# Performance work log

Measured on AMD Instinct MI355X. Metric: run time of the kernel, lower is better.

Reference implementation:

```python
import jax, jax.numpy as jnp
import numpy as np

S, B, H, V, U = 512, 16, 256, 10000, 10000
LAMBDA_T = 0.1   # flashback default temporal decay
LAMBDA_S = 100.0 # flashback default spatial decay
DAY = 86400.0


def setup_inputs() -> dict:
    key = jax.random.key(0)
    ks = jax.random.split(key, 16)
    x = jax.random.randint(ks[0], (S, B), 0, V)
    t = jax.random.uniform(ks[1], (S, B), jnp.float32) * (7.0 * DAY)  # timestamps in seconds
    s = jax.random.normal(ks[2], (S, B, 2), jnp.float32)              # lat/lon-like coords
    y_t = jax.random.uniform(ks[3], (S, B), jnp.float32)
    y_s = jax.random.normal(ks[4], (S, B, 2), jnp.float32)
    h = jnp.zeros((2, B, H), jnp.float32)
    active_user = jax.random.randint(ks[5], (1, B), 0, U)
    sc = 0.02
    enc_emb = jax.random.normal(ks[6], (V, H), jnp.float32) * sc
    user_emb = jax.random.normal(ks[7], (U, H), jnp.float32) * sc
    Wih_f = jax.random.normal(ks[8], (H, H), jnp.float32) * sc
    Whh_f = jax.random.normal(ks[9], (H, H), jnp.float32) * sc
    b_f = jnp.zeros((H,), jnp.float32)
    Wih_b = jax.random.normal(ks[10], (H, H), jnp.float32) * sc
    Whh_b = jax.random.normal(ks[11], (H, H), jnp.float32) * sc
    b_b = jnp.zeros((H,), jnp.float32)
    fc_W = jax.random.normal(ks[12], (V, 3 * H), jnp.float32) * sc
    fc_b = jnp.zeros((V,), jnp.float32)
    return dict(x=x, t=t, s=s, y_t=y_t, y_s=y_s, h=h, active_user=active_user,
                enc_emb=enc_emb, user_emb=user_emb,
                Wih_f=Wih_f, Whh_f=Whh_f, b_f=b_f,
                Wih_b=Wih_b, Whh_b=Whh_b, b_b=b_b,
                fc_W=fc_W, fc_b=fc_b)


def _rnn_dir(xe, h0, Wih, Whh, b):
    # vanilla tanh RNN over leading (time) axis; xe: [S,B,H]
    def step(hprev, xt):
        hn = jnp.tanh(xt @ Wih.T + hprev @ Whh.T + b)
        return hn, hn
    hT, ys = jax.lax.scan(step, h0, xe)
    return ys, hT


def _forward(x, t, s, h, active_user, enc_emb, user_emb,
             Wih_f, Whh_f, b_f, Wih_b, Whh_b, b_b, fc_W, fc_b):
    seq_len, user_len = x.shape
    x_emb = enc_emb[x]                           # [S,B,H]
    out_f, h_f = _rnn_dir(x_emb, h[0], Wih_f, Whh_f, b_f)
    out_b_rev, h_b = _rnn_dir(x_emb[::-1], h[1], Wih_b, Whh_b, b_b)
    h_out = jnp.stack([h_f, h_b], 0)             # [2,B,H]

    # pairwise causal decay weights (i = query step, j = key step, j <= i)
    dt = t[:, None, :] - t[None, :, :]           # [S,S,B]
    ds = jnp.sqrt(jnp.sum((s[:, None] - s[None, :]) ** 2, axis=-1))  # [S,S,B]
    a = ((jnp.cos(dt * (2.0 * np.pi / DAY)) + 1.0) * 0.5) * jnp.exp(-(dt / DAY) * LAMBDA_T)
    b_w = jnp.exp(-ds * LAMBDA_S)
    w = a * b_w + 1e-10                          # [S,S,B]
    causal = jnp.tril(jnp.ones((seq_len, seq_len), w.dtype))
    w = w * causal[:, :, None]
    sum_w = jnp.sum(w, axis=1)                   # [S,B]
    out_w_forward = jnp.einsum('ijb,jbh->ibh', w, out_f) / sum_w[:, :, None]
    # NOTE: original code has a bug (accumulates out_w_backward into itself),
    # so out_w_backward is identically zero; reproduce faithfully.
    out_w_backward = jnp.zeros_like(out_w_forward)

    out_w = jnp.concatenate([out_w_forward, out_w_backward], axis=2)  # [S,B,2H]
    ow = jnp.transpose(out_w, (1, 0, 2))         # [B,S,2H]
    # dropout is identity in eval mode -> query == out_w
    scores = jnp.einsum('bqd,bkd->bqk', ow, ow) / jnp.sqrt(jnp.asarray(2 * H, ow.dtype))
    alpha = jax.nn.softmax(scores, axis=-1)
    ctx = jnp.einsum('bqk,bkd->bqd', alpha, ow)  # [B,S,2H]
    attn_output = jnp.transpose(ctx, (1, 0, 2))  # [S,B,2H]

    p_u = user_emb[active_user.reshape(user_len)]            # [B,H]
    p_u_b = jnp.broadcast_to(p_u[None], (seq_len, user_len, H))
    out_pu = jnp.concatenate([attn_output, p_u_b], axis=2)   # [S,B,3H]
    y_linear = out_pu @ fc_W.T + fc_b                        # [S,B,V]
    return y_linear, h_out


def reference(x, t, s, y_t, y_s, h, active_user, enc_emb, user_emb,
              Wih_f, Whh_f, b_f, Wih_b, Whh_b, b_b, fc_W, fc_b):
    return _forward(x, t, s, h, active_user, enc_emb, user_emb,
                    Wih_f, Whh_f, b_f, Wih_b, Whh_b, b_b, fc_W, fc_b)
```

## Files before the change

### kernel.cpp

```cpp
#include <hip/hip_runtime.h>

typedef unsigned short ushort_t;
typedef __attribute__((ext_vector_type(8))) short short8;
typedef __attribute__((ext_vector_type(4))) float f32x4;

#define S_LEN 512
#define NB 16
#define NH 256
#define NV 10000

__device__ __forceinline__ unsigned short f2bf(float f){
  unsigned u = __float_as_uint(f);
  u += 0x7fffu + ((u >> 16) & 1u);
  return (unsigned short)(u >> 16);
}


__global__ __launch_bounds__(256) void k_prep_xemb(const int* __restrict__ x,
    const float* __restrict__ emb, ushort_t* __restrict__ xe, ushort_t* __restrict__ xer){
  int g = blockIdx.x * 256 + threadIdx.x;
  int m = g >> 5, c = (g & 31) << 3;
  int xm = x[m];
  const float* src = emb + (size_t)xm * NH + c;
  float4 a = *(const float4*)src, b = *(const float4*)(src + 4);
  union { ushort_t us[8]; uint4 v; } u;
  u.us[0]=f2bf(a.x); u.us[1]=f2bf(a.y); u.us[2]=f2bf(a.z); u.us[3]=f2bf(a.w);
  u.us[4]=f2bf(b.x); u.us[5]=f2bf(b.y); u.us[6]=f2bf(b.z); u.us[7]=f2bf(b.w);
  int s = m >> 4, bidx = m & 15;
  int mr = ((S_LEN - 1 - s) << 4) | bidx;
  *(uint4*)&xe [(size_t)m  * NH + c] = u.v;
  *(uint4*)&xer[(size_t)mr * NH + c] = u.v;
}

__global__ __launch_bounds__(256) void k_cvt(const float* __restrict__ src,
                                             ushort_t* __restrict__ dst, int n){
  int g = (blockIdx.x * 256 + threadIdx.x) * 8;
  if (g >= n) return;
  float4 a = *(const float4*)(src + g), b = *(const float4*)(src + g + 4);
  union { ushort_t us[8]; uint4 v; } u;
  u.us[0]=f2bf(a.x); u.us[1]=f2bf(a.y); u.us[2]=f2bf(a.z); u.us[3]=f2bf(a.w);
  u.us[4]=f2bf(b.x); u.us[5]=f2bf(b.y); u.us[6]=f2bf(b.z); u.us[7]=f2bf(b.w);
  *(uint4*)&dst[g] = u.v;
}

__global__ __launch_bounds__(256) void k_prep_fcw(const float* __restrict__ fcW,
                                                  ushort_t* __restrict__ out){
  int g = blockIdx.x * 256 + threadIdx.x;
  int v = g >> 5, c = (g & 31) << 3;
  union { ushort_t us[8]; uint4 q; } u;
  if (v < NV){
    const float* p = fcW + (size_t)v * 768 + c;
    float4 a = *(const float4*)p, b = *(const float4*)(p + 4);
    u.us[0]=f2bf(a.x); u.us[1]=f2bf(a.y); u.us[2]=f2bf(a.z); u.us[3]=f2bf(a.w);
    u.us[4]=f2bf(b.x); u.us[5]=f2bf(b.y); u.us[6]=f2bf(b.z); u.us[7]=f2bf(b.w);
  } else {
    u.q = make_uint4(0,0,0,0);
  }
  *(uint4*)&out[(size_t)v * NH + c] = u.q;
}

__global__ __launch_bounds__(256) void k_prep_tsT(const float* __restrict__ t,
    const float* __restrict__ s2, float* __restrict__ tT,
    float* __restrict__ sxT, float* __restrict__ syT){
  int g = blockIdx.x * 256 + threadIdx.x;
  int j = g >> 4, b = g & 15;
  tT [b * S_LEN + j] = t[g];
  sxT[b * S_LEN + j] = s2[(size_t)g * 2];
  syT[b * S_LEN + j] = s2[(size_t)g * 2 + 1];
}

__global__ __launch_bounds__(256) void k_prep_w(const float* __restrict__ tT,
    const float* __restrict__ sxT, const float* __restrict__ syT,
    ushort_t* __restrict__ wb, float* __restrict__ rsum){
  int i = blockIdx.x, b = blockIdx.y, tid = threadIdx.x;
  const float C1 = 7.272205216643040e-05f;
  const float C2 = -1.1574074074074074e-06f;
  float ti = tT[b*S_LEN+i], sxi = sxT[b*S_LEN+i], syi = syT[b*S_LEN+i];
  __shared__ float red[256];
  float psum = 0.f;
  #pragma unroll
  for (int u2 = 0; u2 < 2; u2++){
    int j = tid + u2 * 256;
    float w = 0.f;
    if (j <= i){
      float dt = ti - tT[b*S_LEN+j];
      float dx = sxi - sxT[b*S_LEN+j], dy = syi - syT[b*S_LEN+j];
      float ds = sqrtf(dx*dx + dy*dy);
      float a = (__cosf(dt * C1) + 1.f) * 0.5f * __expf(dt * C2);
      float bw = __expf(-100.f * ds);
      w = a * bw + 1e-10f;
    }
    psum += w;
    wb[((size_t)b * S_LEN + i) * S_LEN + j] = f2bf(w);
  }
  red[tid] = psum; __syncthreads();
  for (int st = 128; st > 0; st >>= 1){
    if (tid < st) red[tid] += red[tid + st];
    __syncthreads();
  }
  if (tid == 0) rsum[b * S_LEN + i] = 1.f / red[0];
}

__global__ __launch_bounds__(256) void k_ulog(const int* __restrict__ au,
    const float* __restrict__ uemb, const float* __restrict__ fcW,
    const float* __restrict__ fcb, float* __restrict__ ulog){
  __shared__ float pl[16 * 256];
  int tid = threadIdx.x;
  for (int idx = tid; idx < 16 * 256; idx += 256){
    int b = idx >> 8, hc = idx & 255;
    pl[idx] = uemb[(size_t)au[b] * NH + hc];
  }
  __syncthreads();
  int v = blockIdx.x * 256 + tid;
  if (v >= NV) return;
  float acc[16];
  #pragma unroll
  for (int b = 0; b < 16; b++) acc[b] = 0.f;
  const float* wrow = fcW + (size_t)v * 768 + 512;
  for (int hc = 0; hc < 256; hc += 4){
    float4 w4 = *(const float4*)(wrow + hc);
    #pragma unroll
    for (int b = 0; b < 16; b++){
      acc[b] += w4.x * pl[b*256+hc] + w4.y * pl[b*256+hc+1]
              + w4.z * pl[b*256+hc+2] + w4.w * pl[b*256+hc+3];
    }
  }
  float fb = fcb[v];
  #pragma unroll
  for (int b = 0; b < 16; b++) ulog[(size_t)b * NV + v] = acc[b] + fb;
}

__global__ __launch_bounds__(256) void k_transpose(const ushort_t* __restrict__ src,
    ushort_t* __restrict__ dst, int R, int C, long long sstride, long long dstride){
  __shared__ ushort_t tile[32][33];
  int z = blockIdx.z;
  int c0 = blockIdx.x * 32, r0 = blockIdx.y * 32;
  int tx = threadIdx.x & 31, ty = threadIdx.x >> 5;
  const ushort_t* Sp = src + (size_t)sstride * z;
  ushort_t* Dp = dst + (size_t)dstride * z;
  #pragma unroll
  for (int i = 0; i < 32; i += 8) tile[ty+i][tx] = Sp[(size_t)(r0+ty+i) * C + c0 + tx];
  __syncthreads();
  #pragma unroll
  for (int i = 0; i < 32; i += 8) Dp[(size_t)(c0+ty+i) * R + r0 + tx] = tile[tx][ty+i];
}

__global__ __launch_bounds__(256, 2) void k_gemm(
    const ushort_t* __restrict__ A, const ushort_t* __restrict__ Bt, void* __restrict__ Cp,
    int M, int N, int K, int lda, int ldb, int ldc,
    long long sAz, long long sBz, long long sCz,
    const float* __restrict__ bias,
    const float* __restrict__ rowscale, int rsStride,
    const float* __restrict__ addrow, int ldu,
    float cscale, int cmode){
  __shared__ __align__(16) ushort_t As[128 * 40];
  __shared__ __align__(16) ushort_t Bs[128 * 40];
  int z = blockIdx.z;
  int n0 = blockIdx.x * 128, m0 = blockIdx.y * 128;
  int tid = threadIdx.x;
  int wave = tid >> 6, lane = tid & 63;
  int l15 = lane & 15, q4 = lane >> 4;
  int wm = (wave >> 1) * 64, wn = (wave & 1) * 64;
  const ushort_t* Ab = A + (size_t)sAz * z;
  const ushort_t* Bb = Bt + (size_t)sBz * z;
  int srow = tid >> 1, scol = (tid & 1) * 16;
  f32x4 acc[4][4];
  #pragma unroll
  for (int tm = 0; tm < 4; tm++)
    #pragma unroll
    for (int tn = 0; tn < 4; tn++) acc[tm][tn] = (f32x4){0.f,0.f,0.f,0.f};

  for (int k0 = 0; k0 < K; k0 += 32){
    __syncthreads();
    const ushort_t* ap = Ab + (size_t)(m0+srow)*lda + k0 + scol;
    const ushort_t* bp = Bb + (size_t)(n0+srow)*ldb + k0 + scol;
    *(uint4*)&As[srow*40 + scol]     = *(const uint4*)ap;
    *(uint4*)&As[srow*40 + scol + 8] = *(const uint4*)(ap + 8);
    *(uint4*)&Bs[srow*40 + scol]     = *(const uint4*)bp;
    *(uint4*)&Bs[srow*40 + scol + 8] = *(const uint4*)(bp + 8);
    __syncthreads();
    short8 af[4], bf[4];
    #pragma unroll
    for (int tm = 0; tm < 4; tm++) af[tm] = *(const short8*)&As[(wm + tm*16 + l15)*40 + q4*8];
    #pragma unroll
    for (int tn = 0; tn < 4; tn++) bf[tn] = *(const short8*)&Bs[(wn + tn*16 + l15)*40 + q4*8];
    #pragma unroll
    for (int tm = 0; tm < 4; tm++)
      #pragma unroll
      for (int tn = 0; tn < 4; tn++)
        acc[tm][tn] = __builtin_amdgcn_mfma_f32_16x16x32_bf16(af[tm], bf[tn], acc[tm][tn], 0, 0, 0);
  }

  #pragma unroll
  for (int tm = 0; tm < 4; tm++)
    #pragma unroll
    for (int tn = 0; tn < 4; tn++)
      #pragma unroll
      for (int r = 0; r < 4; r++){
        int mr = m0 + wm + tm*16 + q4*4 + r;
        int nc = n0 + wn + tn*16 + l15;
        if (nc < N){
          float v = acc[tm][tn][r] * cscale;
          if (bias)     v += bias[nc];
          if (rowscale) v *= rowscale[(size_t)z * rsStride + mr];
          if (addrow)   v += addrow[(size_t)(mr & 15) * ldu + nc];
          if (cmode == 0){
            ((float*)Cp)[(size_t)sCz * z + (size_t)mr * ldc + nc] = v;
          } else if (cmode == 1){
            ((ushort_t*)Cp)[(size_t)sCz * z + (size_t)mr * ldc + nc] = f2bf(v);
          } else {
            ((ushort_t*)Cp)[((size_t)mr * 16 + z) * ldc + nc] = f2bf(v);
          }
        }
      }
}

__global__ __launch_bounds__(512, 1) void k_rnn(
    const float* __restrict__ WhhF, const float* __restrict__ WhhB,
    const float* __restrict__ xWf, const float* __restrict__ xWb,
    const float* __restrict__ h0,
    ushort_t* __restrict__ outf,
    float* __restrict__ hout){
  int dir = blockIdx.x >> 1, half = blockIdx.x & 1;
  const float* Whh = dir ? WhhB : WhhF;
  const float* xW  = dir ? xWb : xWf;
  int tid = threadIdx.x, wave = tid >> 6, lane = tid & 63;
  int l15 = lane & 15, q4 = lane >> 4;
  __shared__ __align__(16) ushort_t hl[2][8 * 264];

  for (int idx = tid; idx < 2048; idx += 512){
    int m = idx >> 8, n = idx & 255;
    hl[0][m*264 + n] = f2bf(h0[((size_t)dir * 16 + half * 8 + m) * NH + n]);
  }

  short8 bfr[2][8];
  #pragma unroll
  for (int tn = 0; tn < 2; tn++)
    #pragma unroll
    for (int kk = 0; kk < 8; kk++){
      int n = wave*32 + tn*16 + l15;
      int k = kk*32 + q4*8;
      const float* wp = Whh + (size_t)n * NH + k;
      float4 wa = *(const float4*)wp, wb2 = *(const float4*)(wp + 4);
      short8 f;
      f[0]=(short)f2bf(wa.x); f[1]=(short)f2bf(wa.y); f[2]=(short)f2bf(wa.z); f[3]=(short)f2bf(wa.w);
      f[4]=(short)f2bf(wb2.x); f[5]=(short)f2bf(wb2.y); f[6]=(short)f2bf(wb2.z); f[7]=(short)f2bf(wb2.w);
      bfr[tn][kk] = f;
    }

  int myTn = q4 >> 1;
  int mb   = (q4 & 1) * 4;
  int ncol = wave*32 + myTn*16 + l15;

  const float* xwp = xW + (size_t)(half*8 + mb) * NH + ncol;
  float xwE[4], xwO[4];
  #pragma unroll
  for (int r = 0; r < 4; r++){
    xwE[r] = xwp[r * 256];
    xwO[r] = xwp[r * 256 + 16 * 256];
  }
  xwp += 2 * 16 * 256;

  ushort_t* outp0 = outf + (size_t)(half*8 + mb) * 512 * NH + ncol;
  ushort_t* outp1 = outp0 + (size_t)512 * NH;
  ushort_t* outp2 = outp1 + (size_t)512 * NH;
  ushort_t* outp3 = outp2 + (size_t)512 * NH;

  __syncthreads();

#define RNN_STEP(S_, RB_, WB_, XWU_)                                              \
  {                                                                               \
    short8 af[8];                                                                 \
    _Pragma("unroll")                                                             \
    for (int kk = 0; kk < 8; kk++)                                                \
      af[kk] = *(const short8*)&hl[RB_][(lane & 7)*264 + kk*32 + q4*8];           \
    f32x4 acc0 = (f32x4){0.f,0.f,0.f,0.f}, acc1 = acc0;                           \
    _Pragma("unroll")                                                             \
    for (int kk = 0; kk < 8; kk++){                                               \
      acc0 = __builtin_amdgcn_mfma_f32_16x16x32_bf16(af[kk], bfr[0][kk], acc0, 0,0,0); \
      acc1 = __builtin_amdgcn_mfma_f32_16x16x32_bf16(af[kk], bfr[1][kk], acc1, 0,0,0); \
    }                                                                             \
    f32x4 accS = myTn ? acc1 : acc0;                                              \
    float hv[4];                                                                  \
    _Pragma("unroll")                                                             \
    for (int r = 0; r < 4; r++){                                                  \
      float pre = accS[r] + XWU_[r];                                              \
      float ex = __expf(2.f * pre);                                               \
      hv[r] = 1.f - 2.f * __builtin_amdgcn_rcpf(ex + 1.f);                        \
      hl[WB_][(mb + r)*264 + ncol] = f2bf(hv[r]);                                 \
    }                                                                             \
    if (dir == 0){                                                                \
      outp0[0] = f2bf(hv[0]); outp1[0] = f2bf(hv[1]);                             \
      outp2[0] = f2bf(hv[2]); outp3[0] = f2bf(hv[3]);                             \
      outp0 += 256; outp1 += 256; outp2 += 256; outp3 += 256;                     \
    }                                                                             \
    if ((S_) == 511){                                                             \
      _Pragma("unroll")                                                           \
      for (int r = 0; r < 4; r++)                                                 \
        hout[((size_t)dir*16 + half*8 + mb + r) * NH + ncol] = hv[r];             \
    }                                                                             \
    if ((S_) < 510){                                                              \
      _Pragma("unroll")                                                           \
      for (int r = 0; r < 4; r++) XWU_[r] = xwp[r * 256];                         \
      xwp += 16 * 256;                                                            \
    }                                                                             \
    asm volatile("s_waitcnt lgkmcnt(0)" ::: "memory");                            \
    __builtin_amdgcn_s_barrier();                                                 \
    asm volatile("" ::: "memory");                                                \
  }

  for (int s = 0; s < 512; s += 2){
    RNN_STEP(s,     0, 1, xwE)
    RNN_STEP(s + 1, 1, 0, xwO)
  }
#undef RNN_STEP
}

__global__ __launch_bounds__(256) void k_softmax(const float* __restrict__ sc,
                                                 ushort_t* __restrict__ alpha){
  int q = blockIdx.x, z = blockIdx.y, tid = threadIdx.x;
  const float* row = sc + ((size_t)z * S_LEN + q) * S_LEN;
  float v0 = row[tid], v1 = row[tid + 256];
  __shared__ float red[256];
  red[tid] = fmaxf(v0, v1); __syncthreads();
  for (int st = 128; st > 0; st >>= 1){
    if (tid < st) red[tid] = fmaxf(red[tid], red[tid + st]);
    __syncthreads();
  }
  float mx = red[0]; __syncthreads();
  float e0 = __expf(v0 - mx), e1 = __expf(v1 - mx);
  red[tid] = e0 + e1; __syncthreads();
  for (int st = 128; st > 0; st >>= 1){
    if (tid < st) red[tid] += red[tid + st];
    __syncthreads();
  }
  float inv = 1.f / red[0];
  ushort_t* arow = alpha + ((size_t)z * S_LEN + q) * S_LEN;
  arow[tid]       = f2bf(e0 * inv);
  arow[tid + 256] = f2bf(e1 * inv);
}

extern "C" void kernel_launch(void* const* d_in, const int* in_sizes, int n_in,
                              void* d_out, int out_size, void* d_ws, size_t ws_size,
                              hipStream_t stream){
  const int*   x    = (const int*)d_in[0];
  const float* t    = (const float*)d_in[1];
  const float* s2   = (const float*)d_in[2];
  const float* h0   = (const float*)d_in[5];
  const int*   au   = (const int*)d_in[6];
  const float* emb  = (const float*)d_in[7];
  const float* uemb = (const float*)d_in[8];
  const float* WihF = (const float*)d_in[9];
  const float* WhhF = (const float*)d_in[10];
  const float* bF   = (const float*)d_in[11];
  const float* WihB = (const float*)d_in[12];
  const float* WhhB = (const float*)d_in[13];
  const float* bB   = (const float*)d_in[14];
  const float* fcW  = (const float*)d_in[15];
  const float* fcb  = (const float*)d_in[16];
  float* y    = (float*)d_out;
  float* hout = y + (size_t)S_LEN * NB * NV;

  char* wsc = (char*)d_ws;
  size_t off = 0;
  auto alloc = [&](size_t bytes) -> void* {
    void* p = wsc + off;
    off += (bytes + 255) & ~(size_t)255;
    return p;
  };
  ushort_t* xe    = (ushort_t*)alloc(8192 * 256 * 2);
  ushort_t* xer   = (ushort_t*)alloc(8192 * 256 * 2);
  ushort_t* wihf  = (ushort_t*)alloc(256 * 256 * 2);
  ushort_t* wihb  = (ushort_t*)alloc(256 * 256 * 2);
  float*    xwf   = (float*)alloc((size_t)8192 * 256 * 4);
  float*    xwb   = (float*)alloc((size_t)8192 * 256 * 4);
  ushort_t* outf  = (ushort_t*)alloc((size_t)16 * 512 * 256 * 2);
  ushort_t* outfT = (ushort_t*)alloc((size_t)16 * 256 * 512 * 2);
  ushort_t* wbuf  = (ushort_t*)alloc((size_t)16 * 512 * 512 * 2);
  float*    rsum  = (float*)alloc(16 * 512 * 4);
  ushort_t* owf   = (ushort_t*)alloc((size_t)16 * 512 * 256 * 2);
  ushort_t* owfT  = (ushort_t*)alloc((size_t)16 * 256 * 512 * 2);
  ushort_t* fcw1  = (ushort_t*)alloc((size_t)10112 * 256 * 2);
  float*    ulog  = (float*)alloc((size_t)16 * NV * 4);
  float*    tT    = (float*)alloc(16 * 512 * 4);
  float*    sxT   = (float*)alloc(16 * 512 * 4);
  float*    syT   = (float*)alloc(16 * 512 * 4);
  ushort_t* ctx   = (ushort_t*)alloc((size_t)8192 * 256 * 2);
  float*    scores = xwf;
  ushort_t* alpha  = wbuf;

  k_prep_xemb<<<dim3(1024), dim3(256), 0, stream>>>(x, emb, xe, xer);
  k_cvt<<<dim3(32), dim3(256), 0, stream>>>(WihF, wihf, 65536);
  k_cvt<<<dim3(32), dim3(256), 0, stream>>>(WihB, wihb, 65536);
  k_prep_fcw<<<dim3(1264), dim3(256), 0, stream>>>(fcW, fcw1);
  k_prep_tsT<<<dim3(32), dim3(256), 0, stream>>>(t, s2, tT, sxT, syT);
  k_prep_w<<<dim3(512, 16), dim3(256), 0, stream>>>(tT, sxT, syT, wbuf, rsum);
  k_ulog<<<dim3(40), dim3(256), 0, stream>>>(au, uemb, fcW, fcb, ulog);

  k_gemm<<<dim3(2, 64, 1), dim3(256), 0, stream>>>(xe, wihf, xwf,
      8192, 256, 256, 256, 256, 256, 0, 0, 0, bF, nullptr, 0, nullptr, 0, 1.f, 0);
  k_gemm<<<dim3(2, 64, 1), dim3(256), 0, stream>>>(xer, wihb, xwb,
      8192, 256, 256, 256, 256, 256, 0, 0, 0, bB, nullptr, 0, nullptr, 0, 1.f, 0);

  k_rnn<<<dim3(4), dim3(512), 0, stream>>>(WhhF, WhhB, xwf, xwb, h0, outf, hout);

  k_transpose<<<dim3(8, 16, 16), dim3(256), 0, stream>>>(outf, outfT, 512, 256,
      (long long)512 * 256, (long long)256 * 512);

  k_gemm<<<dim3(2, 4, 16), dim3(256), 0, stream>>>(wbuf, outfT, owf,
      512, 256, 512, 512, 512, 256,
      (long long)512 * 512, (long long)256 * 512, (long long)512 * 256,
      nullptr, rsum, 512, nullptr, 0, 1.f, 1);
  k_transpose<<<dim3(8, 16, 16), dim3(256), 0, stream>>>(owf, owfT, 512, 256,
      (long long)512 * 256, (long long)256 * 512);

  k_gemm<<<dim3(4, 4, 16), dim3(256), 0, stream>>>(owf, owf, scores,
      512, 512, 256, 256, 256, 512,
      (long long)512 * 256, (long long)512 * 256, (long long)512 * 512,
      nullptr, nullptr, 0, nullptr, 0, 0.04419417382415922f, 0);

  k_softmax<<<dim3(512, 16), dim3(256), 0, stream>>>(scores, alpha);

  k_gemm<<<dim3(2, 4, 16), dim3(256), 0, stream>>>(alpha, owfT, ctx,
      512, 256, 512, 512, 512, 256,
      (long long)512 * 512, (long long)256 * 512, 0,
      nullptr, nullptr, 0, nullptr, 0, 1.f, 2);

  k_gemm<<<dim3(79, 64, 1), dim3(256), 0, stream>>>(ctx, fcw1, y,
      8192, 10000, 256, 256, 256, 10000, 0, 0, 0,
      nullptr, nullptr, 0, ulog, 10000, 1.f, 0);
}
```

Baseline: 966.1 us.

## Overlap prep work with serial RNN by fusing into one launch

The serial 4-block RNN kernel now shares a launch with the fc-weight conversion, decay-weight construction and user-embedding conversion blocks, so those independent jobs can fill idle CUs while the recurrence runs. The RNN waves get raised priority and the MFMA accumulation is split into two chains to shorten dependency latency. The user-logit term moves from a scalar FP32 kernel to the bf16 MFMA GEMM, which needs an added row bound check. Buffers are reused (fcw2 aliases xe, pu aliases wihf), so correctness depends on ordering, and the prep blocks may compete with the RNN blocks for resources.

```diff
diff --git a/kernel.cpp b/kernel.cpp
--- a/kernel.cpp
+++ b/kernel.cpp
@@ -15,119 +15,35 @@
   return (unsigned short)(u >> 16);
 }
 
-
-__global__ __launch_bounds__(256) void k_prep_xemb(const int* __restrict__ x,
-    const float* __restrict__ emb, ushort_t* __restrict__ xe, ushort_t* __restrict__ xer){
-  int g = blockIdx.x * 256 + threadIdx.x;
-  int m = g >> 5, c = (g & 31) << 3;
-  int xm = x[m];
-  const float* src = emb + (size_t)xm * NH + c;
-  float4 a = *(const float4*)src, b = *(const float4*)(src + 4);
-  union { ushort_t us[8]; uint4 v; } u;
-  u.us[0]=f2bf(a.x); u.us[1]=f2bf(a.y); u.us[2]=f2bf(a.z); u.us[3]=f2bf(a.w);
-  u.us[4]=f2bf(b.x); u.us[5]=f2bf(b.y); u.us[6]=f2bf(b.z); u.us[7]=f2bf(b.w);
-  int s = m >> 4, bidx = m & 15;
-  int mr = ((S_LEN - 1 - s) << 4) | bidx;
-  *(uint4*)&xe [(size_t)m  * NH + c] = u.v;
-  *(uint4*)&xer[(size_t)mr * NH + c] = u.v;
-}
-
-__global__ __launch_bounds__(256) void k_cvt(const float* __restrict__ src,
-                                             ushort_t* __restrict__ dst, int n){
-  int g = (blockIdx.x * 256 + threadIdx.x) * 8;
-  if (g >= n) return;
+__global__ __launch_bounds__(512) void k_prep0(const int* __restrict__ x,
+    const float* __restrict__ emb, ushort_t* __restrict__ xe, ushort_t* __restrict__ xer,
+    const float* __restrict__ WihF, ushort_t* __restrict__ wihf,
+    const float* __restrict__ WihB, ushort_t* __restrict__ wihb){
+  int bx = blockIdx.x, tid = threadIdx.x;
+  if (bx < 512){
+    int g = bx * 512 + tid;
+    int m = g >> 5, c = (g & 31) << 3;
+    int xm = x[m];
+    const float* src = emb + (size_t)xm * NH + c;
+    float4 a = *(const float4*)src, b = *(const float4*)(src + 4);
+    union { ushort_t us[8]; uint4 v; } u;
+    u.us[0]=f2bf(a.x); u.us[1]=f2bf(a.y); u.us[2]=f2bf(a.z); u.us[3]=f2bf(a.w);
+    u.us[4]=f2bf(b.x); u.us[5]=f2bf(b.y); u.us[6]=f2bf(b.z); u.us[7]=f2bf(b.w);
+    int s = m >> 4, bidx = m & 15;
+    int mr = ((S_LEN - 1 - s) << 4) | bidx;
+    *(uint4*)&xe [(size_t)m  * NH + c] = u.v;
+    *(uint4*)&xer[(size_t)mr * NH + c] = u.v;
+    return;
+  }
+  bx -= 512;
+  const float* src = (bx < 16) ? WihF : WihB;
+  ushort_t* dst = (bx < 16) ? wihf : wihb;
+  int g = ((bx & 15) * 512 + tid) * 8;
   float4 a = *(const float4*)(src + g), b = *(const float4*)(src + g + 4);
   union { ushort_t us[8]; uint4 v; } u;
   u.us[0]=f2bf(a.x); u.us[1]=f2bf(a.y); u.us[2]=f2bf(a.z); u.us[3]=f2bf(a.w);
   u.us[4]=f2bf(b.x); u.us[5]=f2bf(b.y); u.us[6]=f2bf(b.z); u.us[7]=f2bf(b.w);
   *(uint4*)&dst[g] = u.v;
-}
-
-__global__ __launch_bounds__(256) void k_prep_fcw(const float* __restrict__ fcW,
-                                                  ushort_t* __restrict__ out){
-  int g = blockIdx.x * 256 + threadIdx.x;
-  int v = g >> 5, c = (g & 31) << 3;
-  union { ushort_t us[8]; uint4 q; } u;
-  if (v < NV){
-    const float* p = fcW + (size_t)v * 768 + c;
-    float4 a = *(const float4*)p, b = *(const float4*)(p + 4);
-    u.us[0]=f2bf(a.x); u.us[1]=f2bf(a.y); u.us[2]=f2bf(a.z); u.us[3]=f2bf(a.w);
-    u.us[4]=f2bf(b.x); u.us[5]=f2bf(b.y); u.us[6]=f2bf(b.z); u.us[7]=f2bf(b.w);
-  } else {
-    u.q = make_uint4(0,0,0,0);
-  }
-  *(uint4*)&out[(size_t)v * NH + c] = u.q;
-}
-
-__global__ __launch_bounds__(256) void k_prep_tsT(const float* __restrict__ t,
-    const float* __restrict__ s2, float* __restrict__ tT,
-    float* __restrict__ sxT, float* __restrict__ syT){
-  int g = blockIdx.x * 256 + threadIdx.x;
-  int j = g >> 4, b = g & 15;
-  tT [b * S_LEN + j] = t[g];
-  sxT[b * S_LEN + j] = s2[(size_t)g * 2];
-  syT[b * S_LEN + j] = s2[(size_t)g * 2 + 1];
-}
-
-__global__ __launch_bounds__(256) void k_prep_w(const float* __restrict__ tT,
-    const float* __restrict__ sxT, const float* __restrict__ syT,
-    ushort_t* __restrict__ wb, float* __restrict__ rsum){
-  int i = blockIdx.x, b = blockIdx.y, tid = threadIdx.x;
-  const float C1 = 7.272205216643040e-05f;
-  const float C2 = -1.1574074074074074e-06f;
-  float ti = tT[b*S_LEN+i], sxi = sxT[b*S_LEN+i], syi = syT[b*S_LEN+i];
-  __shared__ float red[256];
-  float psum = 0.f;
-  #pragma unroll
-  for (int u2 = 0; u2 < 2; u2++){
-    int j = tid + u2 * 256;
-    float w = 0.f;
-    if (j <= i){
-      float dt = ti - tT[b*S_LEN+j];
-      float dx = sxi - sxT[b*S_LEN+j], dy = syi - syT[b*S_LEN+j];
-      float ds = sqrtf(dx*dx + dy*dy);
-      float a = (__cosf(dt * C1) + 1.f) * 0.5f * __expf(dt * C2);
-      float bw = __expf(-100.f * ds);
-      w = a * bw + 1e-10f;
-    }
-    psum += w;
-    wb[((size_t)b * S_LEN + i) * S_LEN + j] = f2bf(w);
-  }
-  red[tid] = psum; __syncthreads();
-  for (int st = 128; st > 0; st >>= 1){
-    if (tid < st) red[tid] += red[tid + st];
-    __syncthreads();
-  }
-  if (tid == 0) rsum[b * S_LEN + i] = 1.f / red[0];
-}
-
-__global__ __launch_bounds__(256) void k_ulog(const int* __restrict__ au,
-    const float* __restrict__ uemb, const float* __restrict__ fcW,
-    const float* __restrict__ fcb, float* __restrict__ ulog){
-  __shared__ float pl[16 * 256];
-  int tid = threadIdx.x;
-  for (int idx = tid; idx < 16 * 256; idx += 256){
-    int b = idx >> 8, hc = idx & 255;
-    pl[idx] = uemb[(size_t)au[b] * NH + hc];
-  }
-  __syncthreads();
-  int v = blockIdx.x * 256 + tid;
-  if (v >= NV) return;
-  float acc[16];
-  #pragma unroll
-  for (int b = 0; b < 16; b++) acc[b] = 0.f;
-  const float* wrow = fcW + (size_t)v * 768 + 512;
-  for (int hc = 0; hc < 256; hc += 4){
-    float4 w4 = *(const float4*)(wrow + hc);
-    #pragma unroll
-    for (int b = 0; b < 16; b++){
-      acc[b] += w4.x * pl[b*256+hc] + w4.y * pl[b*256+hc+1]
-              + w4.z * pl[b*256+hc+2] + w4.w * pl[b*256+hc+3];
-    }
-  }
-  float fb = fcb[v];
-  #pragma unroll
-  for (int b = 0; b < 16; b++) ulog[(size_t)b * NV + v] = acc[b] + fb;
 }
 
 __global__ __launch_bounds__(256) void k_transpose(const ushort_t* __restrict__ src,
@@ -199,7 +115,7 @@
       for (int r = 0; r < 4; r++){
         int mr = m0 + wm + tm*16 + q4*4 + r;
         int nc = n0 + wn + tn*16 + l15;
-        if (nc < N){
+        if (nc < N && mr < M){
           float v = acc[tm][tn][r] * cscale;
           if (bias)     v += bias[nc];
           if (rowscale) v *= rowscale[(size_t)z * rsStride + mr];
@@ -215,18 +131,89 @@
       }
 }
 
-__global__ __launch_bounds__(512, 1) void k_rnn(
+__global__ __launch_bounds__(512, 1) void k_fused(
     const float* __restrict__ WhhF, const float* __restrict__ WhhB,
     const float* __restrict__ xWf, const float* __restrict__ xWb,
     const float* __restrict__ h0,
     ushort_t* __restrict__ outf,
-    float* __restrict__ hout){
-  int dir = blockIdx.x >> 1, half = blockIdx.x & 1;
+    float* __restrict__ hout,
+    const float* __restrict__ fcW, ushort_t* __restrict__ fcw1, ushort_t* __restrict__ fcw2,
+    const float* __restrict__ t, const float* __restrict__ s2,
+    ushort_t* __restrict__ wb, float* __restrict__ rsum,
+    const int* __restrict__ au, const float* __restrict__ uemb, ushort_t* __restrict__ pu){
+  __shared__ __align__(16) ushort_t hl[2][8 * 264];
+  int bx = blockIdx.x, tid = threadIdx.x;
+
+  if (bx >= 4){
+    int pb = bx - 4;
+    if (pb < 632){
+      int g = pb * 512 + tid;
+      int v = g >> 5, c = (g & 31) << 3;
+      union { ushort_t us[8]; uint4 q; } u1, u2;
+      if (v < NV){
+        const float* p1 = fcW + (size_t)v * 768 + c;
+        const float* p2 = p1 + 512;
+        float4 a1 = *(const float4*)p1, b1 = *(const float4*)(p1 + 4);
+        float4 a2 = *(const float4*)p2, b2 = *(const float4*)(p2 + 4);
+        u1.us[0]=f2bf(a1.x); u1.us[1]=f2bf(a1.y); u1.us[2]=f2bf(a1.z); u1.us[3]=f2bf(a1.w);
+        u1.us[4]=f2bf(b1.x); u1.us[5]=f2bf(b1.y); u1.us[6]=f2bf(b1.z); u1.us[7]=f2bf(b1.w);
+        u2.us[0]=f2bf(a2.x); u2.us[1]=f2bf(a2.y); u2.us[2]=f2bf(a2.z); u2.us[3]=f2bf(a2.w);
+        u2.us[4]=f2bf(b2.x); u2.us[5]=f2bf(b2.y); u2.us[6]=f2bf(b2.z); u2.us[7]=f2bf(b2.w);
+      } else {
+        u1.q = make_uint4(0,0,0,0); u2.q = u1.q;
+      }
+      *(uint4*)&fcw1[(size_t)v * NH + c] = u1.q;
+      *(uint4*)&fcw2[(size_t)v * NH + c] = u2.q;
+      return;
+    }
+    pb -= 632;
+    if (pb < 8192){
+      float* red = (float*)hl;
+      int i = pb >> 4, b = pb & 15, j = tid;
+      const float C1 = 7.272205216643040e-05f;
+      const float C2 = -1.1574074074074074e-06f;
+      float ti  = t[i*16 + b];
+      float sxi = s2[(size_t)(i*16 + b) * 2], syi = s2[(size_t)(i*16 + b) * 2 + 1];
+      float w = 0.f;
+      if (j <= i){
+        float dt = ti - t[j*16 + b];
+        float dx = sxi - s2[(size_t)(j*16 + b) * 2];
+        float dy = syi - s2[(size_t)(j*16 + b) * 2 + 1];
+        float ds = sqrtf(dx*dx + dy*dy);
+        float a = (__cosf(dt * C1) + 1.f) * 0.5f * __expf(dt * C2);
+        float bw = __expf(-100.f * ds);
+        w = a * bw + 1e-10f;
+      }
+      wb[((size_t)b * S_LEN + i) * S_LEN + j] = f2bf(w);
+      red[j] = w; __syncthreads();
+      for (int st = 256; st > 0; st >>= 1){
+        if (j < st) red[j] += red[j + st];
+        __syncthreads();
+      }
+      if (j == 0) rsum[b * S_LEN + i] = 1.f / red[0];
+      return;
+    }
+    pb -= 8192;
+    int g = pb * 512 + tid;
+    int r = g >> 5, c = (g & 31) << 3;
+    union { ushort_t us[8]; uint4 q; } u;
+    if (r < 16){
+      const float* p = uemb + (size_t)au[r] * NH + c;
+      float4 a = *(const float4*)p, b2 = *(const float4*)(p + 4);
+      u.us[0]=f2bf(a.x); u.us[1]=f2bf(a.y); u.us[2]=f2bf(a.z); u.us[3]=f2bf(a.w);
+      u.us[4]=f2bf(b2.x); u.us[5]=f2bf(b2.y); u.us[6]=f2bf(b2.z); u.us[7]=f2bf(b2.w);
+    } else {
+      u.q = make_uint4(0,0,0,0);
+    }
+    *(uint4*)&pu[(size_t)r * NH + c] = u.q;
+    return;
+  }
+
+  int dir = bx >> 1, half = bx & 1;
   const float* Whh = dir ? WhhB : WhhF;
   const float* xW  = dir ? xWb : xWf;
-  int tid = threadIdx.x, wave = tid >> 6, lane = tid & 63;
+  int wave = tid >> 6, lane = tid & 63;
   int l15 = lane & 15, q4 = lane >> 4;
-  __shared__ __align__(16) ushort_t hl[2][8 * 264];
 
   for (int idx = tid; idx < 2048; idx += 512){
     int m = idx >> 8, n = idx & 255;
@@ -266,6 +253,7 @@
   ushort_t* outp2 = outp1 + (size_t)512 * NH;
   ushort_t* outp3 = outp2 + (size_t)512 * NH;
 
+  __builtin_amdgcn_s_setprio(1);
   __syncthreads();
 
 #define RNN_STEP(S_, RB_, WB_, XWU_)                                              \
@@ -274,13 +262,18 @@
     _Pragma("unroll")                                                             \
     for (int kk = 0; kk < 8; kk++)                                                \
       af[kk] = *(const short8*)&hl[RB_][(lane & 7)*264 + kk*32 + q4*8];           \
-    f32x4 acc0 = (f32x4){0.f,0.f,0.f,0.f}, acc1 = acc0;                           \
+    f32x4 a0a = (f32x4){0.f,0.f,0.f,0.f}, a0b = a0a, a1a = a0a, a1b = a0a;        \
     _Pragma("unroll")                                                             \
-    for (int kk = 0; kk < 8; kk++){                                               \
-      acc0 = __builtin_amdgcn_mfma_f32_16x16x32_bf16(af[kk], bfr[0][kk], acc0, 0,0,0); \
-      acc1 = __builtin_amdgcn_mfma_f32_16x16x32_bf16(af[kk], bfr[1][kk], acc1, 0,0,0); \
-    }                                                                             \
-    f32x4 accS = myTn ? acc1 : acc0;                                              \
+    for (int kk = 0; kk < 4; kk++){                                               \
+      a0a = __builtin_amdgcn_mfma_f32_16x16x32_bf16(af[kk], bfr[0][kk], a0a, 0,0,0); \
+      a1a = __builtin_amdgcn_mfma_f32_16x16x32_bf16(af[kk], bfr[1][kk], a1a, 0,0,0); \
+    }                                                                             \
+    _Pragma("unroll")                                                             \
+    for (int kk = 4; kk < 8; kk++){                                               \
+      a0b = __builtin_amdgcn_mfma_f32_16x16x32_bf16(af[kk], bfr[0][kk], a0b, 0,0,0); \
+      a1b = __builtin_amdgcn_mfma_f32_16x16x32_bf16(af[kk], bfr[1][kk], a1b, 0,0,0); \
+    }                                                                             \
+    f32x4 accS = myTn ? (a1a + a1b) : (a0a + a0b);                                \
     float hv[4];                                                                  \
     _Pragma("unroll")                                                             \
     for (int r = 0; r < 4; r++){                                                  \
@@ -382,27 +375,25 @@
   ushort_t* owfT  = (ushort_t*)alloc((size_t)16 * 256 * 512 * 2);
   ushort_t* fcw1  = (ushort_t*)alloc((size_t)10112 * 256 * 2);
   float*    ulog  = (float*)alloc((size_t)16 * NV * 4);
-  float*    tT    = (float*)alloc(16 * 512 * 4);
-  float*    sxT   = (float*)alloc(16 * 512 * 4);
-  float*    syT   = (float*)alloc(16 * 512 * 4);
   ushort_t* ctx   = (ushort_t*)alloc((size_t)8192 * 256 * 2);
   float*    scores = xwf;
   ushort_t* alpha  = wbuf;
-
-  k_prep_xemb<<<dim3(1024), dim3(256), 0, stream>>>(x, emb, xe, xer);
-  k_cvt<<<dim3(32), dim3(256), 0, stream>>>(WihF, wihf, 65536);
-  k_cvt<<<dim3(32), dim3(256), 0, stream>>>(WihB, wihb, 65536);
-  k_prep_fcw<<<dim3(1264), dim3(256), 0, stream>>>(fcW, fcw1);
-  k_prep_tsT<<<dim3(32), dim3(256), 0, stream>>>(t, s2, tT, sxT, syT);
-  k_prep_w<<<dim3(512, 16), dim3(256), 0, stream>>>(tT, sxT, syT, wbuf, rsum);
-  k_ulog<<<dim3(40), dim3(256), 0, stream>>>(au, uemb, fcW, fcb, ulog);
+  ushort_t* fcw2 = xe;
+  ushort_t* pu   = wihf;
+
+  k_prep0<<<dim3(544), dim3(512), 0, stream>>>(x, emb, xe, xer, WihF, wihf, WihB, wihb);
 
   k_gemm<<<dim3(2, 64, 1), dim3(256), 0, stream>>>(xe, wihf, xwf,
       8192, 256, 256, 256, 256, 256, 0, 0, 0, bF, nullptr, 0, nullptr, 0, 1.f, 0);
   k_gemm<<<dim3(2, 64, 1), dim3(256), 0, stream>>>(xer, wihb, xwb,
       8192, 256, 256, 256, 256, 256, 0, 0, 0, bB, nullptr, 0, nullptr, 0, 1.f, 0);
 
-  k_rnn<<<dim3(4), dim3(512), 0, stream>>>(WhhF, WhhB, xwf, xwb, h0, outf, hout);
+  k_fused<<<dim3(4 + 632 + 8192 + 8), dim3(512), 0, stream>>>(
+      WhhF, WhhB, xwf, xwb, h0, outf, hout,
+      fcW, fcw1, fcw2, t, s2, wbuf, rsum, au, uemb, pu);
+
+  k_gemm<<<dim3(79, 1, 1), dim3(256), 0, stream>>>(pu, fcw2, ulog,
+      16, NV, 256, 256, 256, NV, 0, 0, 0, fcb, nullptr, 0, nullptr, 0, 1.f, 0);
 
   k_transpose<<<dim3(8, 16, 16), dim3(256), 0, stream>>>(outf, outfT, 512, 256,
       (long long)512 * 256, (long long)256 * 512);
```

After: 942.8 us. -2.4%, faster.
